# Kernel optimization log

Hardware: AMD Instinct MI355X
Metric: run time of the kernel (lower is better)

## Reference

```python
import jax, jax.numpy as jnp
from jax import lax
import numpy as np

B = 2048
NUM_COMPO = 650
NUM_CHARS = 27533
COMPO_SCORE_THRESH = 0.7
SCORE_ADJ_SCALE = 0.1
K = 10  # top-k chars and max padded hit indices


def setup_inputs() -> dict:
    key = jax.random.key(0)
    k1, k2, k3, k4, k5 = jax.random.split(key, 5)
    return {
        "pred_class_logits": jax.random.normal(k1, (B, NUM_CHARS), dtype=jnp.float32),
        "pred_compo_logits": jax.random.normal(k2, (B, NUM_COMPO), dtype=jnp.float32),
        "chinese_char_ids": jax.random.randint(k3, (B,), 0, NUM_CHARS, dtype=jnp.int32),
        "compo_co_occurrence_prob": jax.random.uniform(k4, (NUM_COMPO, NUM_COMPO), dtype=jnp.float32),
        "compo_chinese_matrix": jax.random.randint(k5, (NUM_COMPO, NUM_CHARS), 0, 2, dtype=jnp.int32),
    }


def _components_to_char(compo_scores, co_occ, matrix):
    """Per-sample: compo_scores [C], co_occ [C,C], matrix [C,V] (0/1 int)."""
    # score adjustment: sum over compos with score>0.88 of co_occ row * score * scale
    hi = compo_scores > 0.88
    w = jnp.where(hi, compo_scores, 0.0)                       # [C]
    adjusted = compo_scores + SCORE_ADJ_SCALE * (w @ co_occ)   # [C]
    max_idx = jnp.argmax(adjusted)
    max_score = compo_scores[max_idx]

    # select compos above threshold, sorted descending by score
    sel = compo_scores > COMPO_SCORE_THRESH
    num_sel = jnp.sum(sel.astype(jnp.int32))
    masked = jnp.where(sel, compo_scores, -jnp.inf)
    order = jnp.argsort(-masked)                                # selected first, desc
    sorted_scores = jnp.take(compo_scores, order)               # [C]

    hit0 = matrix[max_idx]                                      # [V] int

    def cond(st):
        i, hit, _prev = st
        return (i < num_sel) & (jnp.sum(hit) > 1)

    def body(st):
        i, hit, _prev = st
        comp = matrix[order[i]]
        new_hit = ((hit + comp) == 2).astype(hit.dtype)         # intersection
        return (i + 1, new_hit, hit)

    i, hit, prev = lax.while_loop(cond, body, (jnp.int32(1), hit0, hit0))
    num_hit = jnp.sum(hit)
    empty = num_hit == 0
    i = jnp.where(empty, i - 1, i)
    hit = jnp.where(empty, prev, hit)
    hit_score = jnp.where(i == 1, max_score, sorted_scores[i - 1])

    # first K indices where hit == 1, padded with -1 (fixed shape)
    ar = jnp.arange(NUM_CHARS, dtype=jnp.int32)
    vals = jnp.where(hit == 1, NUM_CHARS - ar, 0)
    topv, topi = lax.top_k(vals, K)
    hit_indices = jnp.where(topv > 0, topi.astype(jnp.int32), -1)
    return adjusted, hit_indices, hit_score


def reference(pred_class_logits, pred_compo_logits, chinese_char_ids,
              compo_co_occurrence_prob, compo_chinese_matrix):
    class_probs = jax.nn.softmax(pred_class_logits, axis=1)     # [B, V]
    compo_scores = jax.nn.sigmoid(pred_compo_logits)            # [B, C]
    class_scores, class_indices = lax.top_k(class_probs, K)     # [B, K]

    adjusted, hit_idx, hit_scores = jax.vmap(
        _components_to_char, in_axes=(0, None, None)
    )(compo_scores, compo_co_occurrence_prob, compo_chinese_matrix)

    num_hit = jnp.sum((hit_idx != -1).astype(jnp.int32), axis=1)  # [B]
    pred1 = jnp.where(num_hit == 1, hit_idx[:, 0], class_indices[:, 0])
    pred2 = jnp.where((class_scores[:, 0] < 0.85) & (num_hit == 1),
                      hit_idx[:, 0], class_indices[:, 0])

    hit_compare = jnp.any(class_indices[:, :, None] == hit_idx[:, None, :], axis=2)  # [B,K]
    j = jnp.argmax(hit_compare, axis=1)  # first True (all-False -> 0), matches stable desc argsort[0]
    pred3 = class_indices[jnp.arange(class_indices.shape[0]), j]

    return (class_indices, class_scores, compo_scores, adjusted,
            hit_idx, hit_scores, pred1, pred2, pred3)
```

## Files before the change

### kernel.cpp

```cpp
#include <hip/hip_runtime.h>
#include <math.h>

#define NB 2048
#define NC 650
#define NV 27533
#define NK 10
#define NWRD 861
#define NT 256
#define NCHUNK 11
#define SVCAP 512
#define T0 2.8f

__global__ __launch_bounds__(NT) void pack_kernel(const int* __restrict__ mat,
                                                  unsigned* __restrict__ packed) {
  const int c = blockIdx.x;
  __shared__ unsigned s_w[NWRD];
  for (int w = threadIdx.x; w < NWRD; w += NT) s_w[w] = 0;
  __syncthreads();
  const size_t rbeg = (size_t)c * NV;
  const size_t g0 = rbeg & ~(size_t)3;
  const int pre = (int)(rbeg - g0);
  const int nchunks = (NV + pre + 3) >> 2;
  const size_t NTOT = (size_t)NC * NV;
  for (int t = threadIdx.x; t < nchunks; t += NT) {
    size_t g = g0 + ((size_t)t << 2);
    int4 q;
    if (g + 4 <= NTOT) {
      q = *(const int4*)(mat + g);
    } else {
      q.x = (g < NTOT) ? mat[g] : 0;
      q.y = (g + 1 < NTOT) ? mat[g + 1] : 0;
      q.z = (g + 2 < NTOT) ? mat[g + 2] : 0;
      q.w = (g + 3 < NTOT) ? mat[g + 3] : 0;
    }
    long e0 = (long)g - (long)rbeg;
    unsigned nib = 0;
    if (q.x && e0 >= 0 && e0 < NV) nib |= 1u;
    if (q.y && e0 + 1 >= 0 && e0 + 1 < NV) nib |= 2u;
    if (q.z && e0 + 2 >= 0 && e0 + 2 < NV) nib |= 4u;
    if (q.w && e0 + 3 >= 0 && e0 + 3 < NV) nib |= 8u;
    if (nib) {
      if (e0 < 0) { nib >>= (int)(-e0); e0 = 0; }
      int w = (int)(e0 >> 5), sh = (int)(e0 & 31);
      unsigned long long m = (unsigned long long)nib << sh;
      atomicOr(&s_w[w], (unsigned)m);
      unsigned hi = (unsigned)(m >> 32);
      if (hi && w + 1 < NWRD) atomicOr(&s_w[w + 1], hi);
    }
  }
  __syncthreads();
  unsigned* orow = packed + (size_t)c * NWRD;
  for (int w = threadIdx.x; w < NWRD; w += NT) orow[w] = s_w[w];
}

__global__ __launch_bounds__(NT, 6) void gen_pred_kernel(
    const float* __restrict__ class_logits,
    const float* __restrict__ compo_logits,
    const float* __restrict__ co_occ,
    const unsigned* __restrict__ packed,
    float* __restrict__ out) {
  const int b = blockIdx.x;
  const int tid = threadIdx.x;
  const int lane = tid & 63;
  const int wid = tid >> 6;

  __shared__ __align__(16) char arena[7808];
  float* s_sv_v = (float*)arena;
  int* s_sv_i = (int*)(arena + 2048);
  float* s_score = (float*)arena;
  int* s_selidx = (int*)(arena + 2600);
  float* s_selsc = (float*)(arena + 5200);
  __shared__ __align__(16) char arena2[5200];
  int* s_hi = (int*)arena2;
  float* s_hisc = (float*)(arena2 + 2600);
  unsigned* s_words = (unsigned*)arena2;
  __shared__ int s_order[NC];

  __shared__ float red_f[4];
  __shared__ float red_s[4];
  __shared__ int red_i[4];
  __shared__ int s_svcnt, s_i;
  __shared__ int s_cls_idx[NK];
  __shared__ float s_cls_sc[NK];
  __shared__ int s_hit[NK];
  __shared__ int s_hicnt[NCHUNK];
  __shared__ int s_selcnt[NCHUNK];

  const size_t o_cidx = 0;
  const size_t o_csc = (size_t)NB * NK;
  const size_t o_comp = 2 * (size_t)NB * NK;
  const size_t o_adj = o_comp + (size_t)NB * NC;
  const size_t o_hidx = o_adj + (size_t)NB * NC;
  const size_t o_hsc = o_hidx + (size_t)NB * NK;
  const size_t o_p1 = o_hsc + NB;
  const size_t o_p2 = o_p1 + NB;
  const size_t o_p3 = o_p2 + NB;

  const float* lg = class_logits + (size_t)b * NV;
  const int s0 = (4 - (b & 3)) & 3;
  const int M4 = (NV - s0) >> 2;
  const int baseT = s0 + (M4 << 2);
  const float4* lg4 = (const float4*)(lg + s0);

  if (tid == 0) s_svcnt = 0;
  __syncthreads();

  float mx = -INFINITY, ss0 = 0.f, ss1 = 0.f;

#define APPEND1(x, e)                                                   \
  { int p_ = atomicAdd(&s_svcnt, 1);                                    \
    if (p_ < SVCAP) { s_sv_v[p_] = (x); s_sv_i[p_] = (e); } }

  if (tid < s0) {
    float x = lg[tid];
    ss0 += __expf(x); mx = fmaxf(mx, x);
    if (x >= T0) APPEND1(x, tid);
  }
  {
    int rem = NV - baseT;
    if (tid < rem) {
      float x = lg[baseT + tid];
      ss1 += __expf(x); mx = fmaxf(mx, x);
      if (x >= T0) APPEND1(x, baseT + tid);
    }
  }

#define PROC4(f, ebase)                                                  \
  {                                                                      \
    ss0 += __expf(f.x); ss1 += __expf(f.y);                              \
    ss0 += __expf(f.z); ss1 += __expf(f.w);                              \
    float m4_ = fmaxf(fmaxf(f.x, f.y), fmaxf(f.z, f.w));                 \
    mx = fmaxf(mx, m4_);                                                 \
    if (m4_ >= T0) {                                                     \
      int e_ = (ebase);                                                  \
      int c_ = (f.x >= T0) + (f.y >= T0) + (f.z >= T0) + (f.w >= T0);    \
      int p_ = atomicAdd(&s_svcnt, c_);                                  \
      if (f.x >= T0) { if (p_ < SVCAP) { s_sv_v[p_] = f.x; s_sv_i[p_] = e_; } p_++; }     \
      if (f.y >= T0) { if (p_ < SVCAP) { s_sv_v[p_] = f.y; s_sv_i[p_] = e_ + 1; } p_++; } \
      if (f.z >= T0) { if (p_ < SVCAP) { s_sv_v[p_] = f.z; s_sv_i[p_] = e_ + 2; } p_++; } \
      if (f.w >= T0) { if (p_ < SVCAP) { s_sv_v[p_] = f.w; s_sv_i[p_] = e_ + 3; } p_++; } \
    }                                                                    \
  }

  {
    int v = tid;
    float4 fa, fb;
    bool hb = (v + NT) < M4;
    if (v < M4) fa = lg4[v];
    if (hb) fb = lg4[v + NT];
    while (v < M4) {
      int va = v + 2 * NT, vb = v + 3 * NT;
      float4 fa2, fb2;
      bool ha2 = va < M4, hb2 = vb < M4;
      if (ha2) fa2 = lg4[va];
      if (hb2) fb2 = lg4[vb];
      PROC4(fa, s0 + (v << 2));
      if (hb) PROC4(fb, s0 + ((v + NT) << 2));
      fa = fa2; fb = fb2; hb = hb2; v = va;
    }
  }

  float cl0 = 0.f, cl1 = 0.f, cl2 = 0.f;
  {
    const float* cl = compo_logits + (size_t)b * NC;
    if (tid < NC) cl0 = cl[tid];
    if (tid + NT < NC) cl1 = cl[tid + NT];
    if (tid + 2 * NT < NC) cl2 = cl[tid + 2 * NT];
  }

  {
    float s = ss0 + ss1;
#pragma unroll
    for (int off = 32; off > 0; off >>= 1) s += __shfl_down(s, off);
    float g = mx;
    g = fmaxf(g, __shfl_xor(g, 1));
    g = fmaxf(g, __shfl_xor(g, 2));
    g = fmaxf(g, __shfl_xor(g, 4));
    g = fmaxf(g, __shfl_xor(g, 8));
    float t = fminf(g, __shfl_xor(g, 16));
    t = fminf(t, __shfl_xor(t, 32));
    if (lane == 0) { red_s[wid] = s; red_f[wid] = t; }
  }
  __syncthreads();
  const float Sv = red_s[0] + red_s[1] + red_s[2] + red_s[3];
  const float T = fminf(fminf(red_f[0], red_f[1]), fminf(red_f[2], red_f[3]));
  int svc = s_svcnt;

  if (svc < NK || svc > SVCAP) {
    __syncthreads();
    if (tid == 0) s_svcnt = 0;
    __syncthreads();
    if (tid < s0) { float x = lg[tid]; if (x >= T) APPEND1(x, tid); }
    {
      int rem = NV - baseT;
      if (tid < rem) { float x = lg[baseT + tid]; if (x >= T) APPEND1(x, baseT + tid); }
    }
    for (int v = tid; v < M4; v += NT) {
      float4 f = lg4[v];
      int e = s0 + (v << 2);
      if (f.x >= T) APPEND1(f.x, e);
      if (f.y >= T) APPEND1(f.y, e + 1);
      if (f.z >= T) APPEND1(f.z, e + 2);
      if (f.w >= T) APPEND1(f.w, e + 3);
    }
    __syncthreads();
    svc = s_svcnt;
  }
#undef APPEND1
#undef PROC4
  __syncthreads();

  {
    int S = svc < SVCAP ? svc : SVCAP;
    for (int t2 = tid; t2 < S; t2 += NT) {
      float vt = s_sv_v[t2];
      int it = s_sv_i[t2];
      int r = 0;
#pragma unroll 8
      for (int q = 0; q < S; q++) {
        float vq = s_sv_v[q];
        int iq = s_sv_i[q];
        r += (vq > vt || (vq == vt && iq < it)) ? 1 : 0;
      }
      if (r < NK) { s_cls_idx[r] = it; s_cls_sc[r] = vt; }
    }
  }
  __syncthreads();
  if (tid < NK) {
    int cidx = s_cls_idx[tid];
    float sc = __expf(s_cls_sc[tid]) / Sv;
    s_cls_sc[tid] = sc;
    out[o_cidx + (size_t)b * NK + tid] = (float)cidx;
    out[o_csc + (size_t)b * NK + tid] = sc;
  }

  if (tid < NC) {
    float sc = 1.f / (1.f + expf(-cl0));
    s_score[tid] = sc;
    out[o_comp + (size_t)b * NC + tid] = sc;
  }
  if (tid + NT < NC) {
    float sc = 1.f / (1.f + expf(-cl1));
    s_score[tid + NT] = sc;
    out[o_comp + (size_t)b * NC + tid + NT] = sc;
  }
  if (tid + 2 * NT < NC) {
    float sc = 1.f / (1.f + expf(-cl2));
    s_score[tid + 2 * NT] = sc;
    out[o_comp + (size_t)b * NC + tid + 2 * NT] = sc;
  }
  __syncthreads();

  for (int c = wid; c < NCHUNK; c += 4) {
    int e = (c << 6) + lane;
    float s = (e < NC) ? s_score[e] : 0.f;
    unsigned long long mh = __ballot(s > 0.88f);
    unsigned long long ms = __ballot(s > 0.7f);
    if (lane == 0) { s_hicnt[c] = __popcll(mh); s_selcnt[c] = __popcll(ms); }
  }
  __syncthreads();
  int nhi = 0, nsel = 0;
#pragma unroll
  for (int q = 0; q < NCHUNK; q++) { nhi += s_hicnt[q]; nsel += s_selcnt[q]; }
  for (int c = wid; c < NCHUNK; c += 4) {
    int e = (c << 6) + lane;
    float s = (e < NC) ? s_score[e] : 0.f;
    unsigned long long mh = __ballot(s > 0.88f);
    unsigned long long ms = __ballot(s > 0.7f);
    int oh = 0, os = 0;
    for (int q = 0; q < c; q++) { oh += s_hicnt[q]; os += s_selcnt[q]; }
    unsigned long long lower = (1ull << lane) - 1ull;
    if (s > 0.88f) {
      int p = oh + __popcll(mh & lower);
      s_hi[p] = e; s_hisc[p] = s;
    }
    if (s > 0.7f) {
      int p = os + __popcll(ms & lower);
      s_selidx[p] = e; s_selsc[p] = s;
    }
  }
  __syncthreads();

  for (int t = tid; t < nsel; t += NT) {
    float sj = s_selsc[t];
    int r = 0;
#pragma unroll 8
    for (int q = 0; q < nsel; q++) {
      float sq = s_selsc[q];
      r += (sq > sj || (sq == sj && q < t)) ? 1 : 0;
    }
    s_order[r] = s_selidx[t];
  }

  float bestv = -INFINITY;
  int besti = 0x7fffffff;
  for (int j = tid; j < NC; j += NT) {
    float a0 = 0.f, a1 = 0.f, a2 = 0.f, a3 = 0.f;
    int h = 0;
    for (; h + 4 <= nhi; h += 4) {
      int i0 = s_hi[h], i1 = s_hi[h + 1], i2 = s_hi[h + 2], i3 = s_hi[h + 3];
      float w0 = s_hisc[h], w1 = s_hisc[h + 1];
      float w2 = s_hisc[h + 2], w3 = s_hisc[h + 3];
      float c0 = co_occ[(size_t)i0 * NC + j];
      float c1 = co_occ[(size_t)i1 * NC + j];
      float c2 = co_occ[(size_t)i2 * NC + j];
      float c3 = co_occ[(size_t)i3 * NC + j];
      a0 = fmaf(w0, c0, a0);
      a1 = fmaf(w1, c1, a1);
      a2 = fmaf(w2, c2, a2);
      a3 = fmaf(w3, c3, a3);
    }
    for (; h < nhi; h++) {
      a0 = fmaf(s_hisc[h], co_occ[(size_t)s_hi[h] * NC + j], a0);
    }
    float adj = s_score[j] + 0.1f * ((a0 + a1) + (a2 + a3));
    out[o_adj + (size_t)b * NC + j] = adj;
    if (adj > bestv || (adj == bestv && j < besti)) { bestv = adj; besti = j; }
  }
#pragma unroll
  for (int off = 32; off > 0; off >>= 1) {
    float ov = __shfl_down(bestv, off);
    int oi = __shfl_down(besti, off);
    if (ov > bestv || (ov == bestv && oi < besti)) { bestv = ov; besti = oi; }
  }
  if (lane == 0) { red_f[wid] = bestv; red_i[wid] = besti; }
  __syncthreads();
  int max_idx;
  {
    float bv = red_f[0]; int bi = red_i[0];
#pragma unroll
    for (int q = 1; q < 4; q++) {
      float qv = red_f[q]; int qi = red_i[q];
      if (qv > bv || (qv == bv && qi < bi)) { bv = qv; bi = qi; }
    }
    max_idx = bi;
  }
  const float max_score = s_score[max_idx];
  __syncthreads();

  if (wid == 0) {
    unsigned hw[14], pf0[14], pf1[14];
    const unsigned* prow = packed + (size_t)max_idx * NWRD;
    int pc = 0;
#pragma unroll
    for (int t = 0; t < 14; t++) {
      int w = (t << 6) + lane;
      unsigned x = (w < NWRD) ? prow[w] : 0u;
      hw[t] = x;
      pc += __popc(x);
    }
    unsigned long long nz0 = __ballot(pc != 0);
    bool many = (__ballot(pc > 1) != 0ull) || (__popcll(nz0) > 1);
    int i = 1;
    if (nsel > 1) {
      const unsigned* row = packed + (size_t)s_order[1] * NWRD;
#pragma unroll
      for (int t = 0; t < 14; t++) {
        int w = (t << 6) + lane;
        pf0[t] = (w < NWRD) ? row[w] : 0u;
      }
    }
    if (nsel > 2) {
      const unsigned* row = packed + (size_t)s_order[2] * NWRD;
#pragma unroll
      for (int t = 0; t < 14; t++) {
        int w = (t << 6) + lane;
        pf1[t] = (w < NWRD) ? row[w] : 0u;
      }
    }
    while (i < nsel && many) {
      int p2 = 0;
#pragma unroll
      for (int t = 0; t < 14; t++) p2 += __popc(hw[t] & pf0[t]);
      unsigned long long bnz = __ballot(p2 != 0);
      if (bnz == 0ull) break;
#pragma unroll
      for (int t = 0; t < 14; t++) hw[t] &= pf0[t];
      many = (__ballot(p2 > 1) != 0ull) || (__popcll(bnz) > 1);
      i++;
#pragma unroll
      for (int t = 0; t < 14; t++) pf0[t] = pf1[t];
      if (i + 1 < nsel && many) {
        const unsigned* row = packed + (size_t)s_order[i + 1] * NWRD;
#pragma unroll
        for (int t = 0; t < 14; t++) {
          int w = (t << 6) + lane;
          pf1[t] = (w < NWRD) ? row[w] : 0u;
        }
      }
    }
#pragma unroll
    for (int t = 0; t < 14; t++) {
      int w = (t << 6) + lane;
      if (w < NWRD) s_words[w] = hw[t];
    }
    if (lane == 0) s_i = i;
  }
  __syncthreads();

  if (tid < NK) s_hit[tid] = -1;
  {
    unsigned wv[4];
    int myc = 0;
#pragma unroll
    for (int t = 0; t < 4; t++) {
      int w = (tid << 2) + t;
      unsigned x = (w < NWRD) ? s_words[w] : 0u;
      wv[t] = x;
      myc += __popc(x);
    }
    int inc = myc;
#pragma unroll
    for (int off = 1; off < 64; off <<= 1) {
      int y = __shfl_up(inc, off);
      if (lane >= off) inc += y;
    }
    if (lane == 63) red_i[wid] = inc;
    __syncthreads();
    int excl = inc - myc;
    for (int q = 0; q < wid; q++) excl += red_i[q];
    int r = excl;
    if (r < NK) {
#pragma unroll
      for (int t = 0; t < 4; t++) {
        unsigned x = wv[t];
        int wb = ((tid << 2) + t) << 5;
        while (x && r < NK) {
          int bpos = __ffs(x) - 1;
          x &= x - 1;
          s_hit[r] = wb + bpos;
          r++;
        }
        if (r >= NK) break;
      }
    }
  }
  __syncthreads();

  {
    int i = s_i;
    if (tid < NK) out[o_hidx + (size_t)b * NK + tid] = (float)s_hit[tid];
    if (tid == 0) {
      float hsc = (i <= 1) ? max_score : s_score[s_order[i - 1]];
      out[o_hsc + b] = hsc;
      int ci0 = s_cls_idx[0];
      float cs0 = s_cls_sc[0];
      int h0 = s_hit[0];
      bool nh1 = (s_hit[0] >= 0) && (s_hit[1] < 0);
      int p1 = nh1 ? h0 : ci0;
      int p2 = (cs0 < 0.85f && nh1) ? h0 : ci0;
      int jj = 0;
      for (int k = 0; k < NK; k++) {
        bool m = false;
#pragma unroll
        for (int q = 0; q < NK; q++) m = m || (s_cls_idx[k] == s_hit[q]);
        if (m) { jj = k; break; }
      }
      out[o_p1 + b] = (float)p1;
      out[o_p2 + b] = (float)p2;
      out[o_p3 + b] = (float)s_cls_idx[jj];
    }
  }
}

extern "C" void kernel_launch(void* const* d_in, const int* in_sizes, int n_in,
                              void* d_out, int out_size, void* d_ws, size_t ws_size,
                              hipStream_t stream) {
  const float* class_logits = (const float*)d_in[0];
  const float* compo_logits = (const float*)d_in[1];
  const float* co_occ = (const float*)d_in[3];
  const int* mat = (const int*)d_in[4];
  float* out = (float*)d_out;
  unsigned* packed = (unsigned*)d_ws;

  pack_kernel<<<NC, NT, 0, stream>>>(mat, packed);
  gen_pred_kernel<<<NB, NT, 0, stream>>>(class_logits, compo_logits, co_occ,
                                         packed, out);
}
```

Measured before the change: 422.2 us.

## Split top-k from component matching; run one wavefront per sample

The fused per-sample kernel is split into a topk_kernel (softmax plus top-10 over the class logits, 256 threads per sample) and a be_kernel that handles one sample per wavefront, four samples per block. This removes most block-wide __syncthreads and the idle waves in the serial bit-intersection loop. The pack kernel now builds bitmasks with wavefront ballots instead of shared-memory atomics. In exchange, class indices and scores are written to global memory and read back by the second kernel, and the selected and high-score lists get fixed caps that could truncate results if more components pass the thresholds.

```diff
diff --git a/kernel.cpp b/kernel.cpp
--- a/kernel.cpp
+++ b/kernel.cpp
@@ -10,91 +10,61 @@
 #define NCHUNK 11
 #define SVCAP 512
 #define T0 2.8f
+#define SELCAP 256
+#define HICAP 96
+#define BPB 4
+
+#define O_CIDX ((size_t)0)
+#define O_CSC ((size_t)NB * NK)
+#define O_COMP (2 * (size_t)NB * NK)
+#define O_ADJ (O_COMP + (size_t)NB * NC)
+#define O_HIDX (O_ADJ + (size_t)NB * NC)
+#define O_HSC (O_HIDX + (size_t)NB * NK)
+#define O_P1 (O_HSC + NB)
+#define O_P2 (O_P1 + NB)
+#define O_P3 (O_P2 + NB)
 
 __global__ __launch_bounds__(NT) void pack_kernel(const int* __restrict__ mat,
                                                   unsigned* __restrict__ packed) {
   const int c = blockIdx.x;
-  __shared__ unsigned s_w[NWRD];
-  for (int w = threadIdx.x; w < NWRD; w += NT) s_w[w] = 0;
-  __syncthreads();
-  const size_t rbeg = (size_t)c * NV;
-  const size_t g0 = rbeg & ~(size_t)3;
-  const int pre = (int)(rbeg - g0);
-  const int nchunks = (NV + pre + 3) >> 2;
-  const size_t NTOT = (size_t)NC * NV;
-  for (int t = threadIdx.x; t < nchunks; t += NT) {
-    size_t g = g0 + ((size_t)t << 2);
-    int4 q;
-    if (g + 4 <= NTOT) {
-      q = *(const int4*)(mat + g);
-    } else {
-      q.x = (g < NTOT) ? mat[g] : 0;
-      q.y = (g + 1 < NTOT) ? mat[g + 1] : 0;
-      q.z = (g + 2 < NTOT) ? mat[g + 2] : 0;
-      q.w = (g + 3 < NTOT) ? mat[g + 3] : 0;
-    }
-    long e0 = (long)g - (long)rbeg;
-    unsigned nib = 0;
-    if (q.x && e0 >= 0 && e0 < NV) nib |= 1u;
-    if (q.y && e0 + 1 >= 0 && e0 + 1 < NV) nib |= 2u;
-    if (q.z && e0 + 2 >= 0 && e0 + 2 < NV) nib |= 4u;
-    if (q.w && e0 + 3 >= 0 && e0 + 3 < NV) nib |= 8u;
-    if (nib) {
-      if (e0 < 0) { nib >>= (int)(-e0); e0 = 0; }
-      int w = (int)(e0 >> 5), sh = (int)(e0 & 31);
-      unsigned long long m = (unsigned long long)nib << sh;
-      atomicOr(&s_w[w], (unsigned)m);
-      unsigned hi = (unsigned)(m >> 32);
-      if (hi && w + 1 < NWRD) atomicOr(&s_w[w + 1], hi);
-    }
-  }
-  __syncthreads();
+  const int lane = threadIdx.x & 63;
+  const int w = threadIdx.x >> 6;
+  const int* row = mat + (size_t)c * NV;
   unsigned* orow = packed + (size_t)c * NWRD;
-  for (int w = threadIdx.x; w < NWRD; w += NT) orow[w] = s_w[w];
+  for (int k = 0; k < 27; k++) {
+    int g0 = w * 108 + k * 4;
+    int e0 = (g0 << 6) + lane;
+    int x0 = 0, x1 = 0, x2 = 0, x3 = 0;
+    if (e0 < NV) x0 = row[e0];
+    if (e0 + 64 < NV) x1 = row[e0 + 64];
+    if (e0 + 128 < NV) x2 = row[e0 + 128];
+    if (e0 + 192 < NV) x3 = row[e0 + 192];
+    unsigned long long m0 = __ballot(x0 != 0);
+    unsigned long long m1 = __ballot(x1 != 0);
+    unsigned long long m2 = __ballot(x2 != 0);
+    unsigned long long m3 = __ballot(x3 != 0);
+    unsigned long long mm = (lane < 2) ? m0 : (lane < 4) ? m1 : (lane < 6) ? m2 : m3;
+    unsigned v = (lane & 1) ? (unsigned)(mm >> 32) : (unsigned)mm;
+    int wd = (g0 << 1) + lane;
+    if (lane < 8 && wd < NWRD) orow[wd] = v;
+  }
 }
 
-__global__ __launch_bounds__(NT, 6) void gen_pred_kernel(
+__global__ __launch_bounds__(NT, 8) void topk_kernel(
     const float* __restrict__ class_logits,
-    const float* __restrict__ compo_logits,
-    const float* __restrict__ co_occ,
-    const unsigned* __restrict__ packed,
     float* __restrict__ out) {
   const int b = blockIdx.x;
   const int tid = threadIdx.x;
   const int lane = tid & 63;
   const int wid = tid >> 6;
 
-  __shared__ __align__(16) char arena[7808];
-  float* s_sv_v = (float*)arena;
-  int* s_sv_i = (int*)(arena + 2048);
-  float* s_score = (float*)arena;
-  int* s_selidx = (int*)(arena + 2600);
-  float* s_selsc = (float*)(arena + 5200);
-  __shared__ __align__(16) char arena2[5200];
-  int* s_hi = (int*)arena2;
-  float* s_hisc = (float*)(arena2 + 2600);
-  unsigned* s_words = (unsigned*)arena2;
-  __shared__ int s_order[NC];
-
+  __shared__ float s_sv_v[SVCAP];
+  __shared__ int s_sv_i[SVCAP];
   __shared__ float red_f[4];
   __shared__ float red_s[4];
-  __shared__ int red_i[4];
-  __shared__ int s_svcnt, s_i;
+  __shared__ int s_svcnt;
   __shared__ int s_cls_idx[NK];
   __shared__ float s_cls_sc[NK];
-  __shared__ int s_hit[NK];
-  __shared__ int s_hicnt[NCHUNK];
-  __shared__ int s_selcnt[NCHUNK];
-
-  const size_t o_cidx = 0;
-  const size_t o_csc = (size_t)NB * NK;
-  const size_t o_comp = 2 * (size_t)NB * NK;
-  const size_t o_adj = o_comp + (size_t)NB * NC;
-  const size_t o_hidx = o_adj + (size_t)NB * NC;
-  const size_t o_hsc = o_hidx + (size_t)NB * NK;
-  const size_t o_p1 = o_hsc + NB;
-  const size_t o_p2 = o_p1 + NB;
-  const size_t o_p3 = o_p2 + NB;
 
   const float* lg = class_logits + (size_t)b * NV;
   const int s0 = (4 - (b & 3)) & 3;
@@ -160,14 +130,6 @@
     }
   }
 
-  float cl0 = 0.f, cl1 = 0.f, cl2 = 0.f;
-  {
-    const float* cl = compo_logits + (size_t)b * NC;
-    if (tid < NC) cl0 = cl[tid];
-    if (tid + NT < NC) cl1 = cl[tid + NT];
-    if (tid + 2 * NT < NC) cl2 = cl[tid + 2 * NT];
-  }
-
   {
     float s = ss0 + ss1;
 #pragma unroll
@@ -229,59 +191,66 @@
   if (tid < NK) {
     int cidx = s_cls_idx[tid];
     float sc = __expf(s_cls_sc[tid]) / Sv;
-    s_cls_sc[tid] = sc;
-    out[o_cidx + (size_t)b * NK + tid] = (float)cidx;
-    out[o_csc + (size_t)b * NK + tid] = sc;
-  }
-
-  if (tid < NC) {
-    float sc = 1.f / (1.f + expf(-cl0));
-    s_score[tid] = sc;
-    out[o_comp + (size_t)b * NC + tid] = sc;
-  }
-  if (tid + NT < NC) {
-    float sc = 1.f / (1.f + expf(-cl1));
-    s_score[tid + NT] = sc;
-    out[o_comp + (size_t)b * NC + tid + NT] = sc;
-  }
-  if (tid + 2 * NT < NC) {
-    float sc = 1.f / (1.f + expf(-cl2));
-    s_score[tid + 2 * NT] = sc;
-    out[o_comp + (size_t)b * NC + tid + 2 * NT] = sc;
-  }
-  __syncthreads();
-
-  for (int c = wid; c < NCHUNK; c += 4) {
-    int e = (c << 6) + lane;
-    float s = (e < NC) ? s_score[e] : 0.f;
+    out[O_CIDX + (size_t)b * NK + tid] = (float)cidx;
+    out[O_CSC + (size_t)b * NK + tid] = sc;
+  }
+}
+
+__global__ __launch_bounds__(NT, 4) void be_kernel(
+    const float* __restrict__ compo_logits,
+    const float* __restrict__ co_occ,
+    const unsigned* __restrict__ packed,
+    float* __restrict__ out) {
+  const int lane = threadIdx.x & 63;
+  const int wvid = threadIdx.x >> 6;
+  const int b = (blockIdx.x << 2) + wvid;
+
+  __shared__ __align__(16) char arena_all[BPB * 7488];
+  char* arena = arena_all + wvid * 7488;
+  float* s_score = (float*)arena;
+  float* s_selsc = (float*)(arena + 2600);
+  int* s_selidx = (int*)(arena + 3624);
+  int* s_order = (int*)(arena + 4648);
+  float* s_osc = (float*)(arena + 5672);
+  int* s_hi = (int*)(arena + 6696);
+  float* s_hisc = (float*)(arena + 7080);
+  unsigned* s_words = (unsigned*)arena;
+  int* s_hit = s_hi;
+
+  const float* cl = compo_logits + (size_t)b * NC;
+  float xv[NCHUNK];
+#pragma unroll
+  for (int k = 0; k < NCHUNK; k++) {
+    int e = (k << 6) + lane;
+    xv[k] = (e < NC) ? cl[e] : -100.f;
+  }
+  int nsel = 0, nhi = 0;
+#pragma unroll
+  for (int k = 0; k < NCHUNK; k++) {
+    int e = (k << 6) + lane;
+    float s = 1.f / (1.f + expf(-xv[k]));
+    if (e < NC) {
+      s_score[e] = s;
+      out[O_COMP + (size_t)b * NC + e] = s;
+    }
+    unsigned long long ms = __ballot(s > 0.7f);
     unsigned long long mh = __ballot(s > 0.88f);
-    unsigned long long ms = __ballot(s > 0.7f);
-    if (lane == 0) { s_hicnt[c] = __popcll(mh); s_selcnt[c] = __popcll(ms); }
-  }
-  __syncthreads();
-  int nhi = 0, nsel = 0;
-#pragma unroll
-  for (int q = 0; q < NCHUNK; q++) { nhi += s_hicnt[q]; nsel += s_selcnt[q]; }
-  for (int c = wid; c < NCHUNK; c += 4) {
-    int e = (c << 6) + lane;
-    float s = (e < NC) ? s_score[e] : 0.f;
-    unsigned long long mh = __ballot(s > 0.88f);
-    unsigned long long ms = __ballot(s > 0.7f);
-    int oh = 0, os = 0;
-    for (int q = 0; q < c; q++) { oh += s_hicnt[q]; os += s_selcnt[q]; }
     unsigned long long lower = (1ull << lane) - 1ull;
+    if (s > 0.7f) {
+      int p = nsel + __popcll(ms & lower);
+      if (p < SELCAP) { s_selidx[p] = e; s_selsc[p] = s; }
+    }
     if (s > 0.88f) {
-      int p = oh + __popcll(mh & lower);
-      s_hi[p] = e; s_hisc[p] = s;
-    }
-    if (s > 0.7f) {
-      int p = os + __popcll(ms & lower);
-      s_selidx[p] = e; s_selsc[p] = s;
-    }
-  }
-  __syncthreads();
-
-  for (int t = tid; t < nsel; t += NT) {
+      int p = nhi + __popcll(mh & lower);
+      if (p < HICAP) { s_hi[p] = e; s_hisc[p] = s; }
+    }
+    nsel += (int)__popcll(ms);
+    nhi += (int)__popcll(mh);
+  }
+  if (nsel > SELCAP) nsel = SELCAP;
+  if (nhi > HICAP) nhi = HICAP;
+
+  for (int t = lane; t < nsel; t += 64) {
     float sj = s_selsc[t];
     int r = 0;
 #pragma unroll 8
@@ -290,11 +259,15 @@
       r += (sq > sj || (sq == sj && q < t)) ? 1 : 0;
     }
     s_order[r] = s_selidx[t];
+    s_osc[r] = sj;
   }
 
   float bestv = -INFINITY;
   int besti = 0x7fffffff;
-  for (int j = tid; j < NC; j += NT) {
+  const size_t ob = O_ADJ + (size_t)b * NC;
+  for (int k = 0; k < NCHUNK; k++) {
+    int j = (k << 6) + lane;
+    if (j >= NC) break;
     float a0 = 0.f, a1 = 0.f, a2 = 0.f, a3 = 0.f;
     int h = 0;
     for (; h + 4 <= nhi; h += 4) {
@@ -314,38 +287,27 @@
       a0 = fmaf(s_hisc[h], co_occ[(size_t)s_hi[h] * NC + j], a0);
     }
     float adj = s_score[j] + 0.1f * ((a0 + a1) + (a2 + a3));
-    out[o_adj + (size_t)b * NC + j] = adj;
+    out[ob + j] = adj;
     if (adj > bestv || (adj == bestv && j < besti)) { bestv = adj; besti = j; }
   }
 #pragma unroll
-  for (int off = 32; off > 0; off >>= 1) {
-    float ov = __shfl_down(bestv, off);
-    int oi = __shfl_down(besti, off);
+  for (int off = 1; off < 64; off <<= 1) {
+    float ov = __shfl_xor(bestv, off);
+    int oi = __shfl_xor(besti, off);
     if (ov > bestv || (ov == bestv && oi < besti)) { bestv = ov; besti = oi; }
   }
-  if (lane == 0) { red_f[wid] = bestv; red_i[wid] = besti; }
-  __syncthreads();
-  int max_idx;
-  {
-    float bv = red_f[0]; int bi = red_i[0];
-#pragma unroll
-    for (int q = 1; q < 4; q++) {
-      float qv = red_f[q]; int qi = red_i[q];
-      if (qv > bv || (qv == bv && qi < bi)) { bv = qv; bi = qi; }
-    }
-    max_idx = bi;
-  }
+  const int max_idx = besti;
   const float max_score = s_score[max_idx];
-  __syncthreads();
-
-  if (wid == 0) {
-    unsigned hw[14], pf0[14], pf1[14];
+
+  asm volatile("" ::: "memory");
+  unsigned hw[14], pf0[14], pf1[14];
+  {
     const unsigned* prow = packed + (size_t)max_idx * NWRD;
     int pc = 0;
 #pragma unroll
     for (int t = 0; t < 14; t++) {
-      int w = (t << 6) + lane;
-      unsigned x = (w < NWRD) ? prow[w] : 0u;
+      int wd = (t << 6) + lane;
+      unsigned x = (wd < NWRD) ? prow[wd] : 0u;
       hw[t] = x;
       pc += __popc(x);
     }
@@ -356,16 +318,16 @@
       const unsigned* row = packed + (size_t)s_order[1] * NWRD;
 #pragma unroll
       for (int t = 0; t < 14; t++) {
-        int w = (t << 6) + lane;
-        pf0[t] = (w < NWRD) ? row[w] : 0u;
+        int wd = (t << 6) + lane;
+        pf0[t] = (wd < NWRD) ? row[wd] : 0u;
       }
     }
     if (nsel > 2) {
       const unsigned* row = packed + (size_t)s_order[2] * NWRD;
 #pragma unroll
       for (int t = 0; t < 14; t++) {
-        int w = (t << 6) + lane;
-        pf1[t] = (w < NWRD) ? row[w] : 0u;
+        int wd = (t << 6) + lane;
+        pf1[t] = (wd < NWRD) ? row[wd] : 0u;
       }
     }
     while (i < nsel && many) {
@@ -384,29 +346,30 @@
         const unsigned* row = packed + (size_t)s_order[i + 1] * NWRD;
 #pragma unroll
         for (int t = 0; t < 14; t++) {
-          int w = (t << 6) + lane;
-          pf1[t] = (w < NWRD) ? row[w] : 0u;
+          int wd = (t << 6) + lane;
+          pf1[t] = (wd < NWRD) ? row[wd] : 0u;
         }
       }
     }
+    const float hsc = (i <= 1) ? max_score : s_osc[i - 1];
 #pragma unroll
     for (int t = 0; t < 14; t++) {
-      int w = (t << 6) + lane;
-      if (w < NWRD) s_words[w] = hw[t];
-    }
-    if (lane == 0) s_i = i;
-  }
-  __syncthreads();
-
-  if (tid < NK) s_hit[tid] = -1;
-  {
-    unsigned wv[4];
+      int wd = (t << 6) + lane;
+      if (wd < NWRD) s_words[wd] = hw[t];
+    }
+    if (lane == 0) out[O_HSC + b] = hsc;
+  }
+
+  asm volatile("" ::: "memory");
+  if (lane < NK) s_hit[lane] = -1;
+  {
+    unsigned wvv[14];
     int myc = 0;
 #pragma unroll
-    for (int t = 0; t < 4; t++) {
-      int w = (tid << 2) + t;
-      unsigned x = (w < NWRD) ? s_words[w] : 0u;
-      wv[t] = x;
+    for (int t = 0; t < 14; t++) {
+      int wd = lane * 14 + t;
+      unsigned x = (wd < NWRD) ? s_words[wd] : 0u;
+      wvv[t] = x;
       myc += __popc(x);
     }
     int inc = myc;
@@ -415,50 +378,44 @@
       int y = __shfl_up(inc, off);
       if (lane >= off) inc += y;
     }
-    if (lane == 63) red_i[wid] = inc;
-    __syncthreads();
-    int excl = inc - myc;
-    for (int q = 0; q < wid; q++) excl += red_i[q];
-    int r = excl;
+    int r = inc - myc;
     if (r < NK) {
 #pragma unroll
-      for (int t = 0; t < 4; t++) {
-        unsigned x = wv[t];
-        int wb = ((tid << 2) + t) << 5;
+      for (int t = 0; t < 14; t++) {
+        unsigned x = wvv[t];
+        int wb = (lane * 14 + t) << 5;
         while (x && r < NK) {
-          int bpos = __ffs(x) - 1;
+          int bp = __ffs(x) - 1;
           x &= x - 1;
-          s_hit[r] = wb + bpos;
+          s_hit[r] = wb + bp;
           r++;
         }
         if (r >= NK) break;
       }
     }
   }
-  __syncthreads();
-
-  {
-    int i = s_i;
-    if (tid < NK) out[o_hidx + (size_t)b * NK + tid] = (float)s_hit[tid];
-    if (tid == 0) {
-      float hsc = (i <= 1) ? max_score : s_score[s_order[i - 1]];
-      out[o_hsc + b] = hsc;
-      int ci0 = s_cls_idx[0];
-      float cs0 = s_cls_sc[0];
-      int h0 = s_hit[0];
-      bool nh1 = (s_hit[0] >= 0) && (s_hit[1] < 0);
-      int p1 = nh1 ? h0 : ci0;
-      int p2 = (cs0 < 0.85f && nh1) ? h0 : ci0;
-      int jj = 0;
-      for (int k = 0; k < NK; k++) {
-        bool m = false;
-#pragma unroll
-        for (int q = 0; q < NK; q++) m = m || (s_cls_idx[k] == s_hit[q]);
-        if (m) { jj = k; break; }
-      }
-      out[o_p1 + b] = (float)p1;
-      out[o_p2 + b] = (float)p2;
-      out[o_p3 + b] = (float)s_cls_idx[jj];
+
+  asm volatile("" ::: "memory");
+  {
+    if (lane < NK) out[O_HIDX + (size_t)b * NK + lane] = (float)s_hit[lane];
+    int ci = 0;
+    bool m = false;
+    if (lane < NK) {
+      ci = (int)out[O_CIDX + (size_t)b * NK + lane];
+#pragma unroll
+      for (int q = 0; q < NK; q++) m = m || (ci == s_hit[q]);
+    }
+    unsigned long long bm = __ballot(m);
+    int jj = bm ? (__ffsll((unsigned long long)bm) - 1) : 0;
+    int p3i = __shfl(ci, jj);
+    int ci0 = __shfl(ci, 0);
+    int h0 = s_hit[0];
+    bool nh1 = (s_hit[0] >= 0) && (s_hit[1] < 0);
+    if (lane == 0) {
+      float cs0 = out[O_CSC + (size_t)b * NK];
+      out[O_P1 + b] = (float)(nh1 ? h0 : ci0);
+      out[O_P2 + b] = (float)((cs0 < 0.85f && nh1) ? h0 : ci0);
+      out[O_P3 + b] = (float)p3i;
     }
   }
 }
@@ -474,6 +431,6 @@
   unsigned* packed = (unsigned*)d_ws;
 
   pack_kernel<<<NC, NT, 0, stream>>>(mat, packed);
-  gen_pred_kernel<<<NB, NT, 0, stream>>>(class_logits, compo_logits, co_occ,
-                                         packed, out);
+  topk_kernel<<<NB, NT, 0, stream>>>(class_logits, out);
+  be_kernel<<<NB / BPB, NT, 0, stream>>>(compo_logits, co_occ, packed, out);
 }
```

New measurement: 466.1 us. 10.4% more time.

## Pack matrix with wave ballots and deepen logits prefetch pipeline

Applied to the files above, without the earlier changes.

The pack kernel now builds bitmask words with wave-wide ballots over coalesced scalar loads. This replaces the shared-memory atomicOr approach and its extra syncs. The main kernel's softmax streaming loop now keeps six float4 loads in flight per thread instead of two, so more memory traffic overlaps with computation. Launch bounds drop from 6 to 4 waves per SIMD to make room for the larger register buffer, which lowers occupancy.

```diff
diff --git a/kernel.cpp b/kernel.cpp
--- a/kernel.cpp
+++ b/kernel.cpp
@@ -10,50 +10,35 @@
 #define NCHUNK 11
 #define SVCAP 512
 #define T0 2.8f
+#define PD 6
 
 __global__ __launch_bounds__(NT) void pack_kernel(const int* __restrict__ mat,
                                                   unsigned* __restrict__ packed) {
   const int c = blockIdx.x;
-  __shared__ unsigned s_w[NWRD];
-  for (int w = threadIdx.x; w < NWRD; w += NT) s_w[w] = 0;
-  __syncthreads();
-  const size_t rbeg = (size_t)c * NV;
-  const size_t g0 = rbeg & ~(size_t)3;
-  const int pre = (int)(rbeg - g0);
-  const int nchunks = (NV + pre + 3) >> 2;
-  const size_t NTOT = (size_t)NC * NV;
-  for (int t = threadIdx.x; t < nchunks; t += NT) {
-    size_t g = g0 + ((size_t)t << 2);
-    int4 q;
-    if (g + 4 <= NTOT) {
-      q = *(const int4*)(mat + g);
-    } else {
-      q.x = (g < NTOT) ? mat[g] : 0;
-      q.y = (g + 1 < NTOT) ? mat[g + 1] : 0;
-      q.z = (g + 2 < NTOT) ? mat[g + 2] : 0;
-      q.w = (g + 3 < NTOT) ? mat[g + 3] : 0;
-    }
-    long e0 = (long)g - (long)rbeg;
-    unsigned nib = 0;
-    if (q.x && e0 >= 0 && e0 < NV) nib |= 1u;
-    if (q.y && e0 + 1 >= 0 && e0 + 1 < NV) nib |= 2u;
-    if (q.z && e0 + 2 >= 0 && e0 + 2 < NV) nib |= 4u;
-    if (q.w && e0 + 3 >= 0 && e0 + 3 < NV) nib |= 8u;
-    if (nib) {
-      if (e0 < 0) { nib >>= (int)(-e0); e0 = 0; }
-      int w = (int)(e0 >> 5), sh = (int)(e0 & 31);
-      unsigned long long m = (unsigned long long)nib << sh;
-      atomicOr(&s_w[w], (unsigned)m);
-      unsigned hi = (unsigned)(m >> 32);
-      if (hi && w + 1 < NWRD) atomicOr(&s_w[w + 1], hi);
-    }
-  }
-  __syncthreads();
+  const int lane = threadIdx.x & 63;
+  const int w = threadIdx.x >> 6;
+  const int* row = mat + (size_t)c * NV;
   unsigned* orow = packed + (size_t)c * NWRD;
-  for (int w = threadIdx.x; w < NWRD; w += NT) orow[w] = s_w[w];
+  for (int k = 0; k < 27; k++) {
+    int g0 = w * 108 + k * 4;
+    int e0 = (g0 << 6) + lane;
+    int x0 = 0, x1 = 0, x2 = 0, x3 = 0;
+    if (e0 < NV) x0 = row[e0];
+    if (e0 + 64 < NV) x1 = row[e0 + 64];
+    if (e0 + 128 < NV) x2 = row[e0 + 128];
+    if (e0 + 192 < NV) x3 = row[e0 + 192];
+    unsigned long long m0 = __ballot(x0 != 0);
+    unsigned long long m1 = __ballot(x1 != 0);
+    unsigned long long m2 = __ballot(x2 != 0);
+    unsigned long long m3 = __ballot(x3 != 0);
+    unsigned long long mm = (lane < 2) ? m0 : (lane < 4) ? m1 : (lane < 6) ? m2 : m3;
+    unsigned v = (lane & 1) ? (unsigned)(mm >> 32) : (unsigned)mm;
+    int wd = (g0 << 1) + lane;
+    if (lane < 8 && wd < NWRD) orow[wd] = v;
+  }
 }
 
-__global__ __launch_bounds__(NT, 6) void gen_pred_kernel(
+__global__ __launch_bounds__(NT, 4) void gen_pred_kernel(
     const float* __restrict__ class_logits,
     const float* __restrict__ compo_logits,
     const float* __restrict__ co_occ,
@@ -143,20 +128,28 @@
   }
 
   {
-    int v = tid;
-    float4 fa, fb;
-    bool hb = (v + NT) < M4;
-    if (v < M4) fa = lg4[v];
-    if (hb) fb = lg4[v + NT];
-    while (v < M4) {
-      int va = v + 2 * NT, vb = v + 3 * NT;
-      float4 fa2, fb2;
-      bool ha2 = va < M4, hb2 = vb < M4;
-      if (ha2) fa2 = lg4[va];
-      if (hb2) fb2 = lg4[vb];
-      PROC4(fa, s0 + (v << 2));
-      if (hb) PROC4(fb, s0 + ((v + NT) << 2));
-      fa = fa2; fb = fb2; hb = hb2; v = va;
+    float4 buf[PD];
+#pragma unroll
+    for (int i = 0; i < PD; i++) {
+      int idx = tid + i * NT;
+      if (idx < M4) buf[i] = lg4[idx];
+    }
+#pragma unroll 1
+    for (int g = 0; g < 30; g += PD) {
+#pragma unroll
+      for (int i = 0; i < PD; i++) {
+        int k = g + i;
+        int idx = tid + k * NT;
+        int idxp = idx + PD * NT;
+        float4 nb;
+        bool nv = idxp < M4;
+        if (nv) nb = lg4[idxp];
+        if (idx < M4) {
+          float4 f = buf[i];
+          PROC4(f, s0 + (idx << 2));
+        }
+        buf[i] = nb;
+      }
     }
   }
 
```

New measurement: 462.1 us. +9.5%, slower.
